# Kernel tuning notes

Hardware: AMD Instinct MI355X
Metric: run time of the kernel (lower is better)

## Reference

```python
import jax, jax.numpy as jnp
import numpy as np
import math

B, H, S, D = 8, 16, 1024, 64


def setup_inputs() -> dict:
    key = jax.random.key(0)
    kq, kk, kv, kl = jax.random.split(key, 4)
    queries = jax.random.normal(kq, (B * H, S, D), dtype=jnp.float32)
    keys = jax.random.normal(kk, (B * H, S, D), dtype=jnp.float32)
    values = jax.random.normal(kv, (B * H, S, D), dtype=jnp.float32)
    valid_lens = jax.random.randint(kl, (B,), 0, 1024, dtype=jnp.int64)
    return {"queries": queries, "keys": keys, "values": values, "valid_lens": valid_lens}


def reference(queries, keys, values, valid_lens):
    d = queries.shape[-1]
    seq_len = queries.shape[1]
    b = valid_lens.shape[0]
    h = queries.shape[0] // b
    scale = 1.0 / math.sqrt(d)
    # [BH, S, S] scores, faithful to bmm(q, k^T)/sqrt(d)
    scores = jnp.einsum("bqd,bkd->bqk", queries, keys) * scale
    # encode_mask: mask[b, q, k] = (k >= valid_lens[b]) for 1-D valid_lens
    key_mask = jnp.arange(seq_len) >= valid_lens[:, None]  # [B, S]
    scores = scores.reshape(b, h, seq_len, seq_len)
    # masked_fill with 1e-6 (NOT -inf), faithful to the original
    scores = jnp.where(key_mask[:, None, None, :], jnp.float32(1e-6), scores)
    attn = jax.nn.softmax(scores, axis=-1)
    out = jnp.einsum("bhqk,bhkd->bhqd", attn, values.reshape(b, h, seq_len, d))
    return out.reshape(b * h, seq_len, d)
```

## Files before the change

kernel.cpp:

```cpp
#include <hip/hip_runtime.h>
#include <hip/hip_bf16.h>

typedef short short4v __attribute__((ext_vector_type(4)));
typedef short short8v __attribute__((ext_vector_type(8)));
typedef float floatx4 __attribute__((ext_vector_type(4)));

#define SLEN 1024
#define DDIM 64
#define NBH  128
#define PSTR 72

__device__ __forceinline__ unsigned short f2bf(float f) {
  union { float f; unsigned int u; } v; v.f = f;
  unsigned int u = v.u;
  u += 0x7fffu + ((u >> 16) & 1u);
  return (unsigned short)(u >> 16);
}

__device__ __forceinline__ unsigned int pkbf(float a, float b) {
  __hip_bfloat162 h = __float22bfloat162_rn(float2{a, b});
  union { __hip_bfloat162 h; unsigned int u; } c; c.h = h;
  return c.u;
}

__device__ __forceinline__ void ld_lds16(const void* g, void* l) {
  __builtin_amdgcn_global_load_lds(
      (const __attribute__((address_space(1))) void*)g,
      (__attribute__((address_space(3))) void*)l, 16, 0, 0);
}

__global__ __launch_bounds__(256)
void prep_k(const float* __restrict__ Kg, unsigned short* __restrict__ wsK) {
  const int t = blockIdx.x * 256 + threadIdx.x;
  const int tile = t >> 9;
  const int q = t & 511;
  const int r = q >> 3, gr = q & 7;
  const float4 f0 = *(const float4*)(Kg + (size_t)t * 8);
  const float4 f1 = *(const float4*)(Kg + (size_t)t * 8 + 4);
  short8v s;
  s[0]=(short)f2bf(f0.x); s[1]=(short)f2bf(f0.y); s[2]=(short)f2bf(f0.z); s[3]=(short)f2bf(f0.w);
  s[4]=(short)f2bf(f1.x); s[5]=(short)f2bf(f1.y); s[6]=(short)f2bf(f1.z); s[7]=(short)f2bf(f1.w);
  *(short8v*)(wsK + (size_t)tile * 4096 + r * 64 + ((gr ^ (r & 7)) * 8)) = s;
}

__global__ __launch_bounds__(256)
void prep_v(const float* __restrict__ Vg, unsigned short* __restrict__ wsVT,
            float* __restrict__ CS) {
  const int w = threadIdx.x >> 6;
  const int d = threadIdx.x & 63;
  const int tile = blockIdx.x * 4 + w;
  const int bh = tile >> 4, ch = tile & 15;
  const float* src = Vg + ((size_t)(bh * SLEN + ch * 64) * DDIM) + d;
  unsigned short* dst = wsVT + (size_t)tile * 4096 + d * 64;
  float sum = 0.f;
  #pragma unroll
  for (int gg = 0; gg < 8; ++gg) {
    short8v s;
    #pragma unroll
    for (int j = 0; j < 8; ++j) {
      const float x = src[(size_t)(gg * 8 + j) * DDIM];
      sum += x;
      s[j] = (short)f2bf(x);
    }
    *(short8v*)(dst + ((gg ^ (d & 7)) * 8)) = s;
  }
  if (CS) CS[(size_t)tile * 64 + d] = sum;
}

__global__ __launch_bounds__(64)
void prep_sv(float* __restrict__ CS) {
  const int bh = blockIdx.x;
  const int d  = threadIdx.x;
  float acc = 0.f;
  for (int ch = 15; ch >= 0; --ch) {
    const size_t idx = ((size_t)bh * 16 + ch) * 64 + d;
    acc += CS[idx];
    CS[idx] = acc;
  }
}

__global__ __launch_bounds__(256)
void attn_main(const float* __restrict__ Qg, const unsigned short* __restrict__ wsK,
               const unsigned short* __restrict__ wsVT, const float* __restrict__ SV,
               const int* __restrict__ vraw, float* __restrict__ Og)
{
  __shared__ unsigned short K_lds[2][4096];
  __shared__ unsigned short VT_lds[2][4096];
  __shared__ unsigned short P_lds[4][32 * PSTR];

  const int t  = threadIdx.x;
  const int w  = t >> 6;
  const int ln = t & 15;
  const int g  = (t >> 4) & 3;
  const int q0 = blockIdx.x * 128;
  const int bh = blockIdx.y;

  int vl;
  {
    const bool is64 = (vraw[1] == 0) && (vraw[3] == 0) && (vraw[5] == 0) && (vraw[7] == 0);
    const int b = bh >> 4;
    vl = is64 ? vraw[2 * b] : vraw[b];
  }
  const int full_ch     = vl >> 6;
  const int has_partial = (vl & 63) ? 1 : 0;
  const int nch         = SV ? (full_ch + has_partial) : 16;
  const int tail_start  = full_ch + has_partial;

  const float qs = 0.125f * 1.44269504f;
  short8v bq[2][2];
  #pragma unroll
  for (int nt = 0; nt < 2; ++nt) {
    const float* qp = Qg + ((size_t)bh * SLEN + q0 + w * 32 + nt * 16 + ln) * DDIM;
    #pragma unroll
    for (int st = 0; st < 2; ++st) {
      const float4 f0 = *(const float4*)(qp + st * 32 + g * 8);
      const float4 f1 = *(const float4*)(qp + st * 32 + g * 8 + 4);
      short8v a;
      a[0]=(short)f2bf(f0.x*qs); a[1]=(short)f2bf(f0.y*qs);
      a[2]=(short)f2bf(f0.z*qs); a[3]=(short)f2bf(f0.w*qs);
      a[4]=(short)f2bf(f1.x*qs); a[5]=(short)f2bf(f1.y*qs);
      a[6]=(short)f2bf(f1.z*qs); a[7]=(short)f2bf(f1.w*qs);
      bq[nt][st] = a;
    }
  }

  const int l7  = ln & 7;
  const int sw0 = ((g) ^ l7) * 8;
  const int sw1 = ((4 + g) ^ l7) * 8;

  short8v ones;
  #pragma unroll
  for (int j = 0; j < 8; ++j) ones[j] = (short)0x3F80;

  floatx4 o[2][4], lacc[2];
  #pragma unroll
  for (int m = 0; m < 2; ++m) {
    lacc[m] = (floatx4){0.f, 0.f, 0.f, 0.f};
    #pragma unroll
    for (int f = 0; f < 4; ++f) o[m][f] = (floatx4){0.f, 0.f, 0.f, 0.f};
  }

  const size_t tbase = (size_t)bh * 16 * 4096;
  auto issue = [&](int ch, int b) {
    const unsigned short* gk = wsK  + tbase + (size_t)ch * 4096;
    const unsigned short* gv = wsVT + tbase + (size_t)ch * 4096;
    ld_lds16(gk + (size_t)t * 8,         &K_lds[b][t * 8]);
    ld_lds16(gk + (size_t)(t + 256) * 8, &K_lds[b][(t + 256) * 8]);
    ld_lds16(gv + (size_t)t * 8,         &VT_lds[b][t * 8]);
    ld_lds16(gv + (size_t)(t + 256) * 8, &VT_lds[b][(t + 256) * 8]);
  };

  if (nch > 0) issue(0, 0);

  for (int ch = 0; ch < nch; ++ch) {
    const int b = ch & 1;
    if (ch + 1 < nch) {
      issue(ch + 1, b ^ 1);
      __builtin_amdgcn_s_waitcnt(0x0f74);
    } else {
      __builtin_amdgcn_s_waitcnt(0x0f70);
    }
    __builtin_amdgcn_s_barrier();

    floatx4 c[4][2];
    #pragma unroll
    for (int mt = 0; mt < 4; ++mt) {
      const short8v a0 = *(const short8v*)&K_lds[b][(mt * 16 + ln) * 64 + sw0];
      const short8v a1 = *(const short8v*)&K_lds[b][(mt * 16 + ln) * 64 + sw1];
      #pragma unroll
      for (int nt = 0; nt < 2; ++nt) {
        floatx4 acc = (floatx4){0.f, 0.f, 0.f, 0.f};
        acc = __builtin_amdgcn_mfma_f32_16x16x32_bf16(a0, bq[nt][0], acc, 0, 0, 0);
        acc = __builtin_amdgcn_mfma_f32_16x16x32_bf16(a1, bq[nt][1], acc, 0, 0, 0);
        c[mt][nt] = acc;
      }
    }

    const bool fullv = (ch < full_ch);
    #pragma unroll
    for (int mt = 0; mt < 4; ++mt) {
      const int kg = ch * 64 + mt * 16 + g * 4;
      #pragma unroll
      for (int nt = 0; nt < 2; ++nt) {
        float p[4];
        if (fullv) {
          #pragma unroll
          for (int i = 0; i < 4; ++i) p[i] = __builtin_amdgcn_exp2f(c[mt][nt][i]);
        } else {
          #pragma unroll
          for (int i = 0; i < 4; ++i) {
            const float x = (kg + i < vl) ? c[mt][nt][i] : 0.0f;
            p[i] = __builtin_amdgcn_exp2f(x);
          }
        }
        union { short4v v; unsigned int u[2]; } pk;
        pk.u[0] = pkbf(p[0], p[1]);
        pk.u[1] = pkbf(p[2], p[3]);
        *(short4v*)&P_lds[w][(nt * 16 + ln) * PSTR + mt * 16 + g * 4] = pk.v;
      }
    }

    #pragma unroll
    for (int st = 0; st < 2; ++st) {
      const short8v ap0 = *(const short8v*)&P_lds[w][(ln)      * PSTR + st * 32 + g * 8];
      const short8v ap1 = *(const short8v*)&P_lds[w][(16 + ln) * PSTR + st * 32 + g * 8];
      lacc[0] = __builtin_amdgcn_mfma_f32_16x16x32_bf16(ap0, ones, lacc[0], 0, 0, 0);
      lacc[1] = __builtin_amdgcn_mfma_f32_16x16x32_bf16(ap1, ones, lacc[1], 0, 0, 0);
      const int sw = (st == 0) ? sw0 : sw1;
      #pragma unroll
      for (int f = 0; f < 4; ++f) {
        const short8v bv = *(const short8v*)&VT_lds[b][(f * 16 + ln) * 64 + sw];
        o[0][f] = __builtin_amdgcn_mfma_f32_16x16x32_bf16(ap0, bv, o[0][f], 0, 0, 0);
        o[1][f] = __builtin_amdgcn_mfma_f32_16x16x32_bf16(ap1, bv, o[1][f], 0, 0, 0);
      }
    }

    if (ch + 1 < nch) __builtin_amdgcn_s_barrier();
  }

  if (SV != nullptr && tail_start < 16) {
    const float* sv = SV + ((size_t)bh * 16 + tail_start) * 64;
    float svf[4];
    #pragma unroll
    for (int f = 0; f < 4; ++f) svf[f] = sv[f * 16 + ln];
    const float ml = (float)(SLEN - tail_start * 64);
    #pragma unroll
    for (int m = 0; m < 2; ++m) {
      #pragma unroll
      for (int i = 0; i < 4; ++i) lacc[m][i] += ml;
      #pragma unroll
      for (int f = 0; f < 4; ++f)
        #pragma unroll
        for (int i = 0; i < 4; ++i) o[m][f][i] += svf[f];
    }
  }

  #pragma unroll
  for (int m = 0; m < 2; ++m) {
    #pragma unroll
    for (int i = 0; i < 4; ++i) {
      const float inv = 1.0f / lacc[m][i];
      const size_t row = (size_t)bh * SLEN + q0 + w * 32 + m * 16 + g * 4 + i;
      #pragma unroll
      for (int f = 0; f < 4; ++f)
        Og[row * DDIM + f * 16 + ln] = o[m][f][i] * inv;
    }
  }
}

#define KSTR 72
__device__ __forceinline__ float bf2f(unsigned short h) {
  union { unsigned int u; float f; } v; v.u = ((unsigned int)h) << 16;
  return v.f;
}
__global__ __launch_bounds__(256)
void attn_fwd_fallback(const float* __restrict__ Qg, const float* __restrict__ Kg,
                       const float* __restrict__ Vg, const int* __restrict__ vraw,
                       float* __restrict__ Og)
{
  __shared__ unsigned short K_lds[64 * KSTR];
  __shared__ unsigned short VT_lds[64 * KSTR];
  __shared__ unsigned short P_lds[4][32 * KSTR];
  const int t  = threadIdx.x;
  const int w  = t >> 6;
  const int ln = t & 15;
  const int g  = (t >> 4) & 3;
  const int q0 = blockIdx.x * 128;
  const int bh = blockIdx.y;
  int vl;
  {
    const bool is64 = (vraw[1] == 0) && (vraw[3] == 0) && (vraw[5] == 0) && (vraw[7] == 0);
    const int b = bh >> 4;
    vl = is64 ? vraw[2 * b] : vraw[b];
  }
  short8v aq[2][2];
  #pragma unroll
  for (int m = 0; m < 2; ++m) {
    const float* qp = Qg + ((size_t)bh * SLEN + q0 + w * 32 + m * 16 + ln) * DDIM;
    #pragma unroll
    for (int st = 0; st < 2; ++st) {
      const int d0 = st * 32 + g * 8;
      const float4 f0 = *(const float4*)(qp + d0);
      const float4 f1 = *(const float4*)(qp + d0 + 4);
      short8v a;
      a[0]=(short)f2bf(f0.x); a[1]=(short)f2bf(f0.y); a[2]=(short)f2bf(f0.z); a[3]=(short)f2bf(f0.w);
      a[4]=(short)f2bf(f1.x); a[5]=(short)f2bf(f1.y); a[6]=(short)f2bf(f1.z); a[7]=(short)f2bf(f1.w);
      aq[m][st] = a;
    }
  }
  float mrow[2][4], lrow[2][4];
  floatx4 o[2][4];
  #pragma unroll
  for (int m = 0; m < 2; ++m) {
    #pragma unroll
    for (int i = 0; i < 4; ++i) { mrow[m][i] = -INFINITY; lrow[m][i] = 0.f; }
    #pragma unroll
    for (int f = 0; f < 4; ++f) o[m][f] = (floatx4){0.f, 0.f, 0.f, 0.f};
  }
  const float scale = 0.125f;
  for (int ch = 0; ch < SLEN / 64; ++ch) {
    const int k0 = ch * 64;
    __syncthreads();
    {
      const int c4 = (t & 15) * 4;
      const int r0 = t >> 4;
      const float* kp = Kg + ((size_t)bh * SLEN + k0 + r0) * DDIM + c4;
      #pragma unroll
      for (int r = 0; r < 4; ++r) {
        const float4 v = *(const float4*)(kp + (size_t)(16 * r) * DDIM);
        short4v bq2;
        bq2[0]=(short)f2bf(v.x); bq2[1]=(short)f2bf(v.y); bq2[2]=(short)f2bf(v.z); bq2[3]=(short)f2bf(v.w);
        *(short4v*)&K_lds[(r0 + 16 * r) * KSTR + c4] = bq2;
      }
    }
    {
      const int kb = (t >> 4) * 4;
      const int db = (t & 15) * 4;
      const float* vp = Vg + ((size_t)bh * SLEN + k0 + kb) * DDIM + db;
      const float4 r0 = *(const float4*)(vp);
      const float4 r1 = *(const float4*)(vp + DDIM);
      const float4 r2 = *(const float4*)(vp + 2 * DDIM);
      const float4 r3 = *(const float4*)(vp + 3 * DDIM);
      short4v wa, wb, wc, wd;
      wa[0]=(short)f2bf(r0.x); wa[1]=(short)f2bf(r1.x); wa[2]=(short)f2bf(r2.x); wa[3]=(short)f2bf(r3.x);
      wb[0]=(short)f2bf(r0.y); wb[1]=(short)f2bf(r1.y); wb[2]=(short)f2bf(r2.y); wb[3]=(short)f2bf(r3.y);
      wc[0]=(short)f2bf(r0.z); wc[1]=(short)f2bf(r1.z); wc[2]=(short)f2bf(r2.z); wc[3]=(short)f2bf(r3.z);
      wd[0]=(short)f2bf(r0.w); wd[1]=(short)f2bf(r1.w); wd[2]=(short)f2bf(r2.w); wd[3]=(short)f2bf(r3.w);
      *(short4v*)&VT_lds[(db + 0) * KSTR + kb] = wa;
      *(short4v*)&VT_lds[(db + 1) * KSTR + kb] = wb;
      *(short4v*)&VT_lds[(db + 2) * KSTR + kb] = wc;
      *(short4v*)&VT_lds[(db + 3) * KSTR + kb] = wd;
    }
    __syncthreads();
    floatx4 c[2][4];
    #pragma unroll
    for (int m = 0; m < 2; ++m)
      #pragma unroll
      for (int f = 0; f < 4; ++f) c[m][f] = (floatx4){0.f, 0.f, 0.f, 0.f};
    #pragma unroll
    for (int f = 0; f < 4; ++f) {
      const short8v b0 = *(const short8v*)&K_lds[(16 * f + ln) * KSTR + g * 8];
      const short8v b1 = *(const short8v*)&K_lds[(16 * f + ln) * KSTR + 32 + g * 8];
      #pragma unroll
      for (int m = 0; m < 2; ++m) {
        c[m][f] = __builtin_amdgcn_mfma_f32_16x16x32_bf16(aq[m][0], b0, c[m][f], 0, 0, 0);
        c[m][f] = __builtin_amdgcn_mfma_f32_16x16x32_bf16(aq[m][1], b1, c[m][f], 0, 0, 0);
      }
    }
    #pragma unroll
    for (int m = 0; m < 2; ++m) {
      float s[4][4];
      #pragma unroll
      for (int f = 0; f < 4; ++f) {
        const int kgl = k0 + 16 * f + ln;
        const bool valid = kgl < vl;
        #pragma unroll
        for (int i = 0; i < 4; ++i)
          s[f][i] = valid ? c[m][f][i] * scale : 1e-6f;
      }
      #pragma unroll
      for (int i = 0; i < 4; ++i) {
        float r = fmaxf(fmaxf(s[0][i], s[1][i]), fmaxf(s[2][i], s[3][i]));
        r = fmaxf(r, __shfl_xor(r, 1));
        r = fmaxf(r, __shfl_xor(r, 2));
        r = fmaxf(r, __shfl_xor(r, 4));
        r = fmaxf(r, __shfl_xor(r, 8));
        const float mn = fmaxf(mrow[m][i], r);
        const float al = __expf(mrow[m][i] - mn);
        mrow[m][i] = mn;
        float rs = 0.f;
        #pragma unroll
        for (int f = 0; f < 4; ++f) {
          const unsigned short pb = f2bf(__expf(s[f][i] - mn));
          P_lds[w][(m * 16 + g * 4 + i) * KSTR + 16 * f + ln] = pb;
          rs += bf2f(pb);
        }
        rs += __shfl_xor(rs, 1);
        rs += __shfl_xor(rs, 2);
        rs += __shfl_xor(rs, 4);
        rs += __shfl_xor(rs, 8);
        lrow[m][i] = lrow[m][i] * al + rs;
        #pragma unroll
        for (int f = 0; f < 4; ++f) o[m][f][i] *= al;
      }
    }
    #pragma unroll
    for (int st = 0; st < 2; ++st) {
      const short8v ap0 = *(const short8v*)&P_lds[w][(ln)*KSTR + st * 32 + g * 8];
      const short8v ap1 = *(const short8v*)&P_lds[w][(16 + ln) * KSTR + st * 32 + g * 8];
      #pragma unroll
      for (int f = 0; f < 4; ++f) {
        const short8v bv = *(const short8v*)&VT_lds[(16 * f + ln) * KSTR + st * 32 + g * 8];
        o[0][f] = __builtin_amdgcn_mfma_f32_16x16x32_bf16(ap0, bv, o[0][f], 0, 0, 0);
        o[1][f] = __builtin_amdgcn_mfma_f32_16x16x32_bf16(ap1, bv, o[1][f], 0, 0, 0);
      }
    }
  }
  #pragma unroll
  for (int m = 0; m < 2; ++m) {
    float inv[4];
    #pragma unroll
    for (int i = 0; i < 4; ++i) inv[i] = 1.0f / lrow[m][i];
    #pragma unroll
    for (int f = 0; f < 4; ++f) {
      #pragma unroll
      for (int i = 0; i < 4; ++i) {
        const size_t row = (size_t)bh * SLEN + q0 + w * 32 + m * 16 + g * 4 + i;
        Og[row * DDIM + 16 * f + ln] = o[m][f][i] * inv[i];
      }
    }
  }
}

extern "C" void kernel_launch(void* const* d_in, const int* in_sizes, int n_in,
                              void* d_out, int out_size, void* d_ws, size_t ws_size,
                              hipStream_t stream) {
  const float* Q = (const float*)d_in[0];
  const float* K = (const float*)d_in[1];
  const float* V = (const float*)d_in[2];
  const int*  vl = (const int*)d_in[3];
  float* out = (float*)d_out;

  const size_t ws_kv = (size_t)2 * NBH * SLEN * DDIM * 2;
  const size_t ws_sv = ws_kv + (size_t)NBH * 16 * 64 * 4;

  if (ws_size >= ws_kv) {
    unsigned short* wsK  = (unsigned short*)d_ws;
    unsigned short* wsVT = wsK + (size_t)NBH * SLEN * DDIM;
    float* CS = (ws_size >= ws_sv) ? (float*)((char*)d_ws + ws_kv) : nullptr;
    prep_k<<<4096, 256, 0, stream>>>(K, wsK);
    prep_v<<<512, 256, 0, stream>>>(V, wsVT, CS);
    if (CS) prep_sv<<<NBH, 64, 0, stream>>>(CS);
    attn_main<<<dim3(SLEN / 128, NBH), dim3(256), 0, stream>>>(Q, wsK, wsVT, CS, vl, out);
  } else {
    attn_fwd_fallback<<<dim3(SLEN / 128, NBH), dim3(256), 0, stream>>>(Q, K, V, vl, out);
  }
}
```

Measured before the change: 175.1 us.

## Fuse prep kernels, schedule batches longest-first, deepen K/V prefetch

Merges the K and V prep kernels into one launch and drops the separate suffix-sum kernel. The attention kernel now sums the chunk sums for the masked tail itself. One prep thread sorts batches by valid length so the attention grid dispatches the longest-work blocks first, which is meant to reduce load imbalance at the end of the grid. The K/V LDS prefetch now issues two chunks ahead before the Q load, and the next refill is issued after the end-of-iteration barrier. The costs are a serial tail sum per block, a tiny sort on one thread, and a larger workspace requirement, since the fast path is taken only when the extra CS and meta space fits.

Measured after the change: 190.5 us. 8.8% more time.

```diff
diff --git a/kernel.cpp b/kernel.cpp
--- a/kernel.cpp
+++ b/kernel.cpp
@@ -30,59 +30,61 @@
 }
 
 __global__ __launch_bounds__(256)
-void prep_k(const float* __restrict__ Kg, unsigned short* __restrict__ wsK) {
-  const int t = blockIdx.x * 256 + threadIdx.x;
-  const int tile = t >> 9;
-  const int q = t & 511;
-  const int r = q >> 3, gr = q & 7;
-  const float4 f0 = *(const float4*)(Kg + (size_t)t * 8);
-  const float4 f1 = *(const float4*)(Kg + (size_t)t * 8 + 4);
-  short8v s;
-  s[0]=(short)f2bf(f0.x); s[1]=(short)f2bf(f0.y); s[2]=(short)f2bf(f0.z); s[3]=(short)f2bf(f0.w);
-  s[4]=(short)f2bf(f1.x); s[5]=(short)f2bf(f1.y); s[6]=(short)f2bf(f1.z); s[7]=(short)f2bf(f1.w);
-  *(short8v*)(wsK + (size_t)tile * 4096 + r * 64 + ((gr ^ (r & 7)) * 8)) = s;
-}
-
-__global__ __launch_bounds__(256)
-void prep_v(const float* __restrict__ Vg, unsigned short* __restrict__ wsVT,
-            float* __restrict__ CS) {
-  const int w = threadIdx.x >> 6;
-  const int d = threadIdx.x & 63;
-  const int tile = blockIdx.x * 4 + w;
-  const int bh = tile >> 4, ch = tile & 15;
-  const float* src = Vg + ((size_t)(bh * SLEN + ch * 64) * DDIM) + d;
-  unsigned short* dst = wsVT + (size_t)tile * 4096 + d * 64;
-  float sum = 0.f;
-  #pragma unroll
-  for (int gg = 0; gg < 8; ++gg) {
+void prep_kv(const float* __restrict__ Kg, const float* __restrict__ Vg,
+             const int* __restrict__ vraw, unsigned short* __restrict__ wsK,
+             unsigned short* __restrict__ wsVT, float* __restrict__ CS,
+             int* __restrict__ meta)
+{
+  const int bid = blockIdx.x;
+  if (bid < 4096) {
+    const int t = bid * 256 + threadIdx.x;
+    const int tile = t >> 9;
+    const int q = t & 511;
+    const int r = q >> 3, gr = q & 7;
+    const float4 f0 = *(const float4*)(Kg + (size_t)t * 8);
+    const float4 f1 = *(const float4*)(Kg + (size_t)t * 8 + 4);
     short8v s;
-    #pragma unroll
-    for (int j = 0; j < 8; ++j) {
-      const float x = src[(size_t)(gg * 8 + j) * DDIM];
-      sum += x;
-      s[j] = (short)f2bf(x);
-    }
-    *(short8v*)(dst + ((gg ^ (d & 7)) * 8)) = s;
-  }
-  if (CS) CS[(size_t)tile * 64 + d] = sum;
-}
-
-__global__ __launch_bounds__(64)
-void prep_sv(float* __restrict__ CS) {
-  const int bh = blockIdx.x;
-  const int d  = threadIdx.x;
-  float acc = 0.f;
-  for (int ch = 15; ch >= 0; --ch) {
-    const size_t idx = ((size_t)bh * 16 + ch) * 64 + d;
-    acc += CS[idx];
-    CS[idx] = acc;
+    s[0]=(short)f2bf(f0.x); s[1]=(short)f2bf(f0.y); s[2]=(short)f2bf(f0.z); s[3]=(short)f2bf(f0.w);
+    s[4]=(short)f2bf(f1.x); s[5]=(short)f2bf(f1.y); s[6]=(short)f2bf(f1.z); s[7]=(short)f2bf(f1.w);
+    *(short8v*)(wsK + (size_t)tile * 4096 + r * 64 + ((gr ^ (r & 7)) * 8)) = s;
+  } else {
+    if (bid == 4096 && threadIdx.x == 0) {
+      const bool is64 = (vraw[1] == 0) && (vraw[3] == 0) && (vraw[5] == 0) && (vraw[7] == 0);
+      int vls[8], ord[8];
+      #pragma unroll
+      for (int b = 0; b < 8; ++b) { vls[b] = is64 ? vraw[2 * b] : vraw[b]; ord[b] = b; }
+      for (int i = 0; i < 8; ++i)
+        for (int j = i + 1; j < 8; ++j)
+          if (vls[ord[j]] > vls[ord[i]]) { int tmp = ord[i]; ord[i] = ord[j]; ord[j] = tmp; }
+      #pragma unroll
+      for (int s = 0; s < 8; ++s) { meta[s] = ord[s]; meta[8 + s] = vls[ord[s]]; }
+    }
+    const int w = threadIdx.x >> 6;
+    const int d = threadIdx.x & 63;
+    const int tile = (bid - 4096) * 4 + w;
+    const int bh = tile >> 4, ch = tile & 15;
+    const float* src = Vg + ((size_t)(bh * SLEN + ch * 64) * DDIM) + d;
+    unsigned short* dst = wsVT + (size_t)tile * 4096 + d * 64;
+    float sum = 0.f;
+    #pragma unroll
+    for (int gg = 0; gg < 8; ++gg) {
+      short8v s;
+      #pragma unroll
+      for (int j = 0; j < 8; ++j) {
+        const float x = src[(size_t)(gg * 8 + j) * DDIM];
+        sum += x;
+        s[j] = (short)f2bf(x);
+      }
+      *(short8v*)(dst + ((gg ^ (d & 7)) * 8)) = s;
+    }
+    CS[(size_t)tile * 64 + d] = sum;
   }
 }
 
 __global__ __launch_bounds__(256)
 void attn_main(const float* __restrict__ Qg, const unsigned short* __restrict__ wsK,
-               const unsigned short* __restrict__ wsVT, const float* __restrict__ SV,
-               const int* __restrict__ vraw, float* __restrict__ Og)
+               const unsigned short* __restrict__ wsVT, const float* __restrict__ CS,
+               const int* __restrict__ meta, float* __restrict__ Og)
 {
   __shared__ unsigned short K_lds[2][4096];
   __shared__ unsigned short VT_lds[2][4096];
@@ -93,18 +95,29 @@
   const int ln = t & 15;
   const int g  = (t >> 4) & 3;
   const int q0 = blockIdx.x * 128;
-  const int bh = blockIdx.y;
-
-  int vl;
-  {
-    const bool is64 = (vraw[1] == 0) && (vraw[3] == 0) && (vraw[5] == 0) && (vraw[7] == 0);
-    const int b = bh >> 4;
-    vl = is64 ? vraw[2 * b] : vraw[b];
-  }
+
+  const int slot  = blockIdx.y >> 4;
+  const int h     = blockIdx.y & 15;
+  const int batch = meta[slot];
+  const int vl    = meta[8 + slot];
+  const int bh    = batch * 16 + h;
+
   const int full_ch     = vl >> 6;
   const int has_partial = (vl & 63) ? 1 : 0;
-  const int nch         = SV ? (full_ch + has_partial) : 16;
-  const int tail_start  = full_ch + has_partial;
+  const int nch         = full_ch + has_partial;
+  const int tail_start  = nch;
+
+  const size_t tbase = (size_t)bh * 16 * 4096;
+  auto issue = [&](int ch, int b) {
+    const unsigned short* gk = wsK  + tbase + (size_t)ch * 4096;
+    const unsigned short* gv = wsVT + tbase + (size_t)ch * 4096;
+    ld_lds16(gk + (size_t)t * 8,         &K_lds[b][t * 8]);
+    ld_lds16(gk + (size_t)(t + 256) * 8, &K_lds[b][(t + 256) * 8]);
+    ld_lds16(gv + (size_t)t * 8,         &VT_lds[b][t * 8]);
+    ld_lds16(gv + (size_t)(t + 256) * 8, &VT_lds[b][(t + 256) * 8]);
+  };
+  if (nch > 0) issue(0, 0);
+  if (nch > 1) issue(1, 1);
 
   const float qs = 0.125f * 1.44269504f;
   short8v bq[2][2];
@@ -140,26 +153,10 @@
     for (int f = 0; f < 4; ++f) o[m][f] = (floatx4){0.f, 0.f, 0.f, 0.f};
   }
 
-  const size_t tbase = (size_t)bh * 16 * 4096;
-  auto issue = [&](int ch, int b) {
-    const unsigned short* gk = wsK  + tbase + (size_t)ch * 4096;
-    const unsigned short* gv = wsVT + tbase + (size_t)ch * 4096;
-    ld_lds16(gk + (size_t)t * 8,         &K_lds[b][t * 8]);
-    ld_lds16(gk + (size_t)(t + 256) * 8, &K_lds[b][(t + 256) * 8]);
-    ld_lds16(gv + (size_t)t * 8,         &VT_lds[b][t * 8]);
-    ld_lds16(gv + (size_t)(t + 256) * 8, &VT_lds[b][(t + 256) * 8]);
-  };
-
-  if (nch > 0) issue(0, 0);
-
   for (int ch = 0; ch < nch; ++ch) {
     const int b = ch & 1;
-    if (ch + 1 < nch) {
-      issue(ch + 1, b ^ 1);
-      __builtin_amdgcn_s_waitcnt(0x0f74);
-    } else {
-      __builtin_amdgcn_s_waitcnt(0x0f70);
-    }
+    if (ch + 1 < nch) __builtin_amdgcn_s_waitcnt(0x0f74);
+    else              __builtin_amdgcn_s_waitcnt(0x0f70);
     __builtin_amdgcn_s_barrier();
 
     floatx4 c[4][2];
@@ -215,14 +212,19 @@
       }
     }
 
-    if (ch + 1 < nch) __builtin_amdgcn_s_barrier();
-  }
-
-  if (SV != nullptr && tail_start < 16) {
-    const float* sv = SV + ((size_t)bh * 16 + tail_start) * 64;
-    float svf[4];
-    #pragma unroll
-    for (int f = 0; f < 4; ++f) svf[f] = sv[f * 16 + ln];
+    if (ch + 2 < nch) {
+      __builtin_amdgcn_s_barrier();
+      issue(ch + 2, b);
+    }
+  }
+
+  if (tail_start < 16) {
+    const float* cs = CS + (size_t)bh * 16 * 64;
+    float svf[4] = {0.f, 0.f, 0.f, 0.f};
+    for (int ch = tail_start; ch < 16; ++ch) {
+      #pragma unroll
+      for (int f = 0; f < 4; ++f) svf[f] += cs[ch * 64 + f * 16 + ln];
+    }
     const float ml = (float)(SLEN - tail_start * 64);
     #pragma unroll
     for (int m = 0; m < 2; ++m) {
@@ -421,17 +423,17 @@
   const int*  vl = (const int*)d_in[3];
   float* out = (float*)d_out;
 
-  const size_t ws_kv = (size_t)2 * NBH * SLEN * DDIM * 2;
-  const size_t ws_sv = ws_kv + (size_t)NBH * 16 * 64 * 4;
-
-  if (ws_size >= ws_kv) {
+  const size_t ws_kv   = (size_t)2 * NBH * SLEN * DDIM * 2;
+  const size_t ws_cs   = (size_t)NBH * 16 * 64 * 4;
+  const size_t ws_need = ws_kv + ws_cs + 64;
+
+  if (ws_size >= ws_need) {
     unsigned short* wsK  = (unsigned short*)d_ws;
     unsigned short* wsVT = wsK + (size_t)NBH * SLEN * DDIM;
-    float* CS = (ws_size >= ws_sv) ? (float*)((char*)d_ws + ws_kv) : nullptr;
-    prep_k<<<4096, 256, 0, stream>>>(K, wsK);
-    prep_v<<<512, 256, 0, stream>>>(V, wsVT, CS);
-    if (CS) prep_sv<<<NBH, 64, 0, stream>>>(CS);
-    attn_main<<<dim3(SLEN / 128, NBH), dim3(256), 0, stream>>>(Q, wsK, wsVT, CS, vl, out);
+    float* CS  = (float*)((char*)d_ws + ws_kv);
+    int*  meta = (int*)((char*)d_ws + ws_kv + ws_cs);
+    prep_kv<<<4608, 256, 0, stream>>>(K, V, vl, wsK, wsVT, CS, meta);
+    attn_main<<<dim3(SLEN / 128, NBH), dim3(256), 0, stream>>>(Q, wsK, wsVT, CS, meta, out);
   } else {
     attn_fwd_fallback<<<dim3(SLEN / 128, NBH), dim3(256), 0, stream>>>(Q, K, V, vl, out);
   }
```
